# Kernel tuning notes

Measured on AMD Instinct MI355X. Metric: run time of the kernel, lower is better.

The kernel has to match this reference:

```python
import jax, jax.numpy as jnp
import numpy as np

NEG_SLOPE = 0.2


def _gatv2_layer(x, Wl, bl, Wr, br, att, bo, src, dst, N):
    """PyG GATv2Conv: lin_l on source, lin_r on target, segment softmax over dst."""
    H, C = att.shape
    xl = (x @ Wl + bl).reshape(N, H, C)  # source transform
    xr = (x @ Wr + br).reshape(N, H, C)  # target transform
    e = jax.nn.leaky_relu(xl[src] + xr[dst], NEG_SLOPE)      # [E,H,C]
    score = jnp.einsum('ehc,hc->eh', e, att)                 # [E,H]
    smax = jax.lax.stop_gradient(
        jax.ops.segment_max(score, dst, num_segments=N))     # [N,H]
    ex = jnp.exp(score - smax[dst])
    denom = jax.ops.segment_sum(ex, dst, num_segments=N)     # [N,H]
    alpha = ex / denom[dst]                                  # [E,H]
    out = jax.ops.segment_sum(xl[src] * alpha[..., None], dst, num_segments=N)
    return out.reshape(N, H * C) + bo, alpha


def setup_inputs() -> dict:
    key = jax.random.key(0)
    ks = jax.random.split(key, 24)
    N, E, F_in, Hd, H = 50000, 800000, 16, 128, 4
    C = Hd // H

    def p(k, shape, scale=0.05):
        return jax.random.normal(k, shape, jnp.float32) * scale

    inp = {
        'x': jax.random.normal(ks[0], (N, F_in), jnp.float32),
        'edge_index': jax.random.randint(ks[1], (2, E), 0, N, jnp.int32),
        'edge_attr': jax.random.normal(ks[2], (E, 4), jnp.float32),
        'batch': jnp.zeros((N,), jnp.int32),
        'enc_W': p(ks[3], (F_in, Hd)), 'enc_b': p(ks[4], (Hd,)),
        'g1_Wl': p(ks[5], (Hd, Hd)), 'g1_bl': p(ks[6], (Hd,)),
        'g1_Wr': p(ks[7], (Hd, Hd)), 'g1_br': p(ks[8], (Hd,)),
        'g1_att': p(ks[9], (H, C)), 'g1_bo': p(ks[10], (Hd,)),
        'g2_Wl': p(ks[11], (Hd, Hd)), 'g2_bl': p(ks[12], (Hd,)),
        'g2_Wr': p(ks[13], (Hd, Hd)), 'g2_br': p(ks[14], (Hd,)),
        'g2_att': p(ks[15], (H, C)), 'g2_bo': p(ks[16], (Hd,)),
        'mlp_W1': p(ks[17], (Hd, Hd)), 'mlp_b1': p(ks[18], (Hd,)),
        'mlp_W2': p(ks[19], (Hd, 1)), 'mlp_b2': p(ks[20], (1,)),
    }
    return inp


def reference(x, edge_index, edge_attr, batch,
              enc_W, enc_b,
              g1_Wl, g1_bl, g1_Wr, g1_br, g1_att, g1_bo,
              g2_Wl, g2_bl, g2_Wr, g2_br, g2_att, g2_bo,
              mlp_W1, mlp_b1, mlp_W2, mlp_b2):
    N = x.shape[0]
    # add_self_loops=True (both GAT layers)
    loops = jnp.arange(N, dtype=edge_index.dtype)
    src = jnp.concatenate([edge_index[0], loops])
    dst = jnp.concatenate([edge_index[1], loops])

    h = x @ enc_W + enc_b                                    # node_encoder
    h1, a1 = _gatv2_layer(h, g1_Wl, g1_bl, g1_Wr, g1_br, g1_att, g1_bo, src, dst, N)
    h1 = jax.nn.relu(h1)
    h2, a2 = _gatv2_layer(h1, g2_Wl, g2_bl, g2_Wr, g2_br, g2_att, g2_bo, src, dst, N)
    logits = jax.nn.relu(h2 @ mlp_W1 + mlp_b1) @ mlp_W2 + mlp_b2  # [N,1]
    probs = jax.nn.sigmoid(logits[:, 0])                     # [N]
    return probs, (a1, a2)
```

## Files before the change

kernel.cpp:

```cpp
#include <hip/hip_runtime.h>
#include <hip/hip_bf16.h>

#define NEG_SLOPE 0.2f
#define AS 136
#define CAPD 64
#define L2E 1.44269504f
#define EPB 4096

typedef __bf16 bf16x8 __attribute__((ext_vector_type(8)));
typedef float  f32x4  __attribute__((ext_vector_type(4)));

__device__ __forceinline__ float b2f(__hip_bfloat16 v) { return __bfloat162float(v); }
__device__ __forceinline__ __hip_bfloat16 f2b(float v) { return __float2bfloat16(v); }
__device__ __forceinline__ float lo16(unsigned u) { return __uint_as_float(u << 16); }
__device__ __forceinline__ float hi16(unsigned u) { return __uint_as_float(u & 0xFFFF0000u); }

template<int CTRL>
__device__ __forceinline__ float dpp_add(float p) {
    int t = __builtin_amdgcn_update_dpp(0, __float_as_int(p), CTRL, 0xF, 0xF, true);
    return p + __int_as_float(t);
}

__device__ __forceinline__ float fexp2(float x) {
    float r;
    asm("v_exp_f32 %0, %1" : "=v"(r) : "v"(x));
    return r;
}

__device__ __forceinline__ int wild16(unsigned short w) {
    int e = (w >> 7) & 0xFF;
    return (e == 0 || e >= 0xC0) ? 1 : 0;
}

__device__ __forceinline__ void store_out(void* out, size_t idx, float v, int isF32) {
    if (isF32) ((float*)out)[idx] = v;
    else       ((__hip_bfloat16*)out)[idx] = f2b(v);
}

#define NCVT 13
struct CvtTab {
    const void* src[NCVT];
    float*      dst[NCVT];
    int         n[NCVT];
    int         total;
};
__global__ void k_cvt_all(CvtTab tab, const unsigned short* __restrict__ det,
                          int* __restrict__ FLAG) {
    __shared__ int sh[256];
    int t = threadIdx.x;
    int cnt = 0;
#pragma unroll
    for (int j = 0; j < 4; ++j) cnt += wild16(det[t * 8 + j * 2]);
    sh[t] = cnt;
    __syncthreads();
    for (int off = 128; off >= 1; off >>= 1) {
        if (t < off) sh[t] += sh[t + off];
        __syncthreads();
    }
    int isF32 = sh[0] > 128;
    if (blockIdx.x == 0 && t == 0) *FLAG = isF32;
    int i = blockIdx.x * blockDim.x + t;
    if (i >= tab.total) return;
    int seg = 0, rem = i;
    while (rem >= tab.n[seg]) { rem -= tab.n[seg]; ++seg; }
    float v = isF32 ? ((const float*)tab.src[seg])[rem]
                    : b2f(((const __hip_bfloat16*)tab.src[seg])[rem]);
    tab.dst[seg][rem] = v;
}

struct WtTab { const void* src[5]; __hip_bfloat16* dst[5]; };
__global__ void k_cvtWt_all(WtTab tab, const unsigned short* __restrict__ det) {
    __shared__ int sh[128];
    int t = threadIdx.x;
    int cnt = 0;
#pragma unroll
    for (int j = 0; j < 8; ++j) cnt += wild16(det[t * 16 + j * 2]);
    sh[t] = cnt;
    __syncthreads();
    for (int off = 64; off >= 1; off >>= 1) {
        if (t < off) sh[t] += sh[t + off];
        __syncthreads();
    }
    int isF32 = sh[0] > 128;
    int m = blockIdx.x >> 7;
    int k = blockIdx.x & 127, c = t;
    float v = isF32 ? ((const float*)tab.src[m])[k * 128 + c]
                    : b2f(((const __hip_bfloat16*)tab.src[m])[k * 128 + c]);
    tab.dst[m][c * 128 + k] = f2b(v);
}


__global__ __launch_bounds__(1024) void k_binA(const int* __restrict__ ei, int E,
        int ET, int N, int shift, int nbkt, int b1, int* __restrict__ gcnt) {
    __shared__ int cnt[1024];
    int t = threadIdx.x, blk = blockIdx.x;
    for (int i = t; i < 1024; i += 1024) cnt[i] = 0;
    __syncthreads();
    int e0 = blk * EPB, e1 = min(e0 + EPB, ET);
    for (int e = e0 + t; e < e1; e += 1024) {
        int d = (e < E) ? ei[E + e] : (e - E);
        if ((unsigned)d < (unsigned)N) atomicAdd(&cnt[d >> shift], 1);
    }
    __syncthreads();
    for (int i = t; i < nbkt; i += 1024) gcnt[(size_t)i * b1 + blk] = cnt[i];
}

__global__ __launch_bounds__(256) void k_scanA(const int* __restrict__ cnt, int M,
                                               int* __restrict__ out, int* __restrict__ bsum) {
    __shared__ int sh[256];
    int t = threadIdx.x, i = blockIdx.x * 256 + t;
    int v = (i < M) ? cnt[i] : 0;
    sh[t] = v;
    __syncthreads();
    for (int off = 1; off < 256; off <<= 1) {
        int u = (t >= off) ? sh[t - off] : 0;
        __syncthreads();
        sh[t] += u;
        __syncthreads();
    }
    if (i < M) out[i] = sh[t] - v;
    if (t == 255) bsum[blockIdx.x] = sh[255];
}

__global__ __launch_bounds__(1024) void k_scanB2(int* __restrict__ bsum, int B,
        int* __restrict__ rs, int N, int* __restrict__ bb, int nbkt) {
    __shared__ int sh[1024];
    int t = threadIdx.x;
    int carry = 0;
    for (int base = 0; base < B; base += 1024) {
        int idx = base + t;
        int v = (idx < B) ? bsum[idx] : 0;
        sh[t] = v;
        __syncthreads();
        for (int off = 1; off < 1024; off <<= 1) {
            int u = (t >= off) ? sh[t - off] : 0;
            __syncthreads();
            sh[t] += u;
            __syncthreads();
        }
        if (idx < B) bsum[idx] = carry + sh[t] - v;
        carry += sh[1023];
        __syncthreads();
    }
    if (t == 0) { rs[N] = carry; bb[nbkt] = carry; }
}

__global__ __launch_bounds__(256) void k_scanC2(int* __restrict__ offs,
        const int* __restrict__ bsum, int M, int b1, int* __restrict__ bb) {
    int i = blockIdx.x * 256 + threadIdx.x;
    if (i >= M) return;
    int v = offs[i] + bsum[blockIdx.x];
    offs[i] = v;
    if (i % b1 == 0) bb[i / b1] = v;
}

__global__ __launch_bounds__(1024) void k_binB(const int* __restrict__ ei, int E,
        int ET, int N, int shift, int nbkt, int b1, const int* __restrict__ offs,
        int2* __restrict__ stg) {
    __shared__ int base[1024];
    int t = threadIdx.x, blk = blockIdx.x;
    for (int i = t; i < nbkt; i += 1024) base[i] = offs[(size_t)i * b1 + blk];
    __syncthreads();
    int mask = (1 << shift) - 1;
    int e0 = blk * EPB, e1 = min(e0 + EPB, ET);
    for (int e = e0 + t; e < e1; e += 1024) {
        int s, d;
        if (e < E) { s = ei[e]; d = ei[E + e]; } else { s = d = e - E; }
        if ((unsigned)d >= (unsigned)N) continue;
        int pos = atomicAdd(&base[d >> shift], 1);
        stg[pos] = make_int2(e, s | ((d & mask) << 20));
    }
}

__global__ __launch_bounds__(256) void k_csr(const int2* __restrict__ stg,
        const int* __restrict__ bb, int N, int shift,
        int* __restrict__ rs, int2* __restrict__ pk) {
    __shared__ int off2[1024];
    __shared__ int cnt2[1024];
    __shared__ int part[256];
    int t = threadIdx.x, bkt = blockIdx.x;
    int node0 = bkt << shift;
    int npb = 1 << shift;
    int mask = npb - 1;
    int nn = min(npb, N - node0);
    int b0 = bb[bkt], bend = bb[bkt + 1];
    int ec = bend - b0;
    const int* stgy = ((const int*)stg) + 1;
    for (int i = t; i < nn; i += 256) cnt2[i] = 0;
    __syncthreads();
    for (int i = t; i < ec; i += 256)
        atomicAdd(&cnt2[(stgy[(size_t)(b0 + i) * 2] >> 20) & mask], 1);
    __syncthreads();
    int loc[4], sum = 0, base4 = t * 4;
#pragma unroll
    for (int k = 0; k < 4; ++k) {
        int idx = base4 + k;
        int v = (idx < nn) ? cnt2[idx] : 0;
        loc[k] = sum; sum += v;
    }
    part[t] = sum;
    __syncthreads();
    for (int off = 1; off < 256; off <<= 1) {
        int u = (t >= off) ? part[t - off] : 0;
        __syncthreads();
        part[t] += u;
        __syncthreads();
    }
    int pbase = part[t] - sum;
#pragma unroll
    for (int k = 0; k < 4; ++k) {
        int idx = base4 + k;
        if (idx < nn) {
            int p = b0 + pbase + loc[k];
            off2[idx] = p;
            rs[node0 + idx] = p;
        }
    }
    __syncthreads();
    for (int i = t; i < ec; i += 256) {
        int2 es = stg[b0 + i];
        int dof = (es.y >> 20) & mask;
        int pos = atomicAdd(&off2[dof], 1);
        pk[pos] = make_int2(es.x, es.y & 0xFFFFF);
    }
}

__global__ __launch_bounds__(256) void k_gemm2enc_mfma(
        const void* __restrict__ x, const float* __restrict__ encW,
        const float* __restrict__ encb, const int* __restrict__ flag,
        const __hip_bfloat16* __restrict__ WLt, const float* __restrict__ bl,
        const __hip_bfloat16* __restrict__ WRt, const float* __restrict__ br,
        int N, __hip_bfloat16* __restrict__ xl, __hip_bfloat16* __restrict__ xr) {
    __shared__ __hip_bfloat16 hA[64 * AS];
    __shared__ __hip_bfloat16 wB[128 * AS];
    float* encWs = (float*)wB;
    float* xs    = encWs + 2048;
    int t = threadIdx.x, rbase = blockIdx.x * 64;
    int isF32 = *flag;
    for (int i = t; i < 2048; i += 256) encWs[i] = encW[i];
    for (int i = t; i < 1024; i += 256) {
        int r = i >> 4, k = i & 15, gr = rbase + r;
        float v = 0.f;
        if (gr < N)
            v = isF32 ? ((const float*)x)[(size_t)gr * 16 + k]
                      : b2f(((const __hip_bfloat16*)x)[(size_t)gr * 16 + k]);
        xs[r * 17 + k] = v;
    }
    __syncthreads();
    {
        int r = t >> 2, q = t & 3;
        float xv[16];
#pragma unroll
        for (int k = 0; k < 16; ++k) xv[k] = xs[r * 17 + k];
#pragma unroll
        for (int cc = 0; cc < 32; ++cc) {
            int c = q + cc * 4;
            float acc = encb[c];
#pragma unroll
            for (int k = 0; k < 16; ++k) acc += xv[k] * encWs[k * 128 + c];
            hA[r * AS + c] = f2b(acc);
        }
    }
    int wave = t >> 6, lane = t & 63, l16 = lane & 15, kq = lane >> 4;
#pragma unroll
    for (int pass = 0; pass < 2; ++pass) {
        const __hip_bfloat16* Wt = pass ? WRt : WLt;
        const float* bias        = pass ? br  : bl;
        __hip_bfloat16* out      = pass ? xr  : xl;
        __syncthreads();
        for (int i = t; i < 2048; i += 256) {
            int c = i >> 4, seg = i & 15;
            ((uint4*)(wB + c * AS))[seg] = ((const uint4*)(Wt + c * 128))[seg];
        }
        __syncthreads();
        f32x4 acc[8];
#pragma unroll
        for (int i = 0; i < 8; ++i) acc[i] = (f32x4){0.f, 0.f, 0.f, 0.f};
#pragma unroll
        for (int ks = 0; ks < 4; ++ks) {
            int kofs = ks * 32 + kq * 8;
            bf16x8 a = *(const bf16x8*)(hA + (wave * 16 + l16) * AS + kofs);
#pragma unroll
            for (int cb = 0; cb < 8; ++cb) {
                bf16x8 b = *(const bf16x8*)(wB + (cb * 16 + l16) * AS + kofs);
                acc[cb] = __builtin_amdgcn_mfma_f32_16x16x32_bf16(a, b, acc[cb], 0, 0, 0);
            }
        }
#pragma unroll
        for (int cb = 0; cb < 8; ++cb) {
            int c = cb * 16 + l16;
            float bc = bias[c];
#pragma unroll
            for (int i = 0; i < 4; ++i) {
                int r = rbase + wave * 16 + kq * 4 + i;
                if (r < N) out[(size_t)r * 128 + c] = f2b(acc[cb][i] + bc);
            }
        }
    }
}

__global__ __launch_bounds__(256) void k_gemm2_mfma(
        const __hip_bfloat16* __restrict__ in,
        const __hip_bfloat16* __restrict__ WLt, const float* __restrict__ bl,
        const __hip_bfloat16* __restrict__ WRt, const float* __restrict__ br,
        int N, __hip_bfloat16* __restrict__ xl, __hip_bfloat16* __restrict__ xr) {
    __shared__ __hip_bfloat16 hA[64 * AS];
    __shared__ __hip_bfloat16 wB[128 * AS];
    int t = threadIdx.x, rbase = blockIdx.x * 64;
    for (int i = t; i < 1024; i += 256) {
        int r = i >> 4, seg = i & 15;
        int gr = rbase + r;
        uint4 v = {0u, 0u, 0u, 0u};
        if (gr < N) v = ((const uint4*)(in + (size_t)gr * 128))[seg];
        ((uint4*)(hA + r * AS))[seg] = v;
    }
    int wave = t >> 6, lane = t & 63, l16 = lane & 15, kq = lane >> 4;
#pragma unroll
    for (int pass = 0; pass < 2; ++pass) {
        const __hip_bfloat16* Wt = pass ? WRt : WLt;
        const float* bias        = pass ? br  : bl;
        __hip_bfloat16* out      = pass ? xr  : xl;
        __syncthreads();
        for (int i = t; i < 2048; i += 256) {
            int c = i >> 4, seg = i & 15;
            ((uint4*)(wB + c * AS))[seg] = ((const uint4*)(Wt + c * 128))[seg];
        }
        __syncthreads();
        f32x4 acc[8];
#pragma unroll
        for (int i = 0; i < 8; ++i) acc[i] = (f32x4){0.f, 0.f, 0.f, 0.f};
#pragma unroll
        for (int ks = 0; ks < 4; ++ks) {
            int kofs = ks * 32 + kq * 8;
            bf16x8 a = *(const bf16x8*)(hA + (wave * 16 + l16) * AS + kofs);
#pragma unroll
            for (int cb = 0; cb < 8; ++cb) {
                bf16x8 b = *(const bf16x8*)(wB + (cb * 16 + l16) * AS + kofs);
                acc[cb] = __builtin_amdgcn_mfma_f32_16x16x32_bf16(a, b, acc[cb], 0, 0, 0);
            }
        }
#pragma unroll
        for (int cb = 0; cb < 8; ++cb) {
            int c = cb * 16 + l16;
            float bc = bias[c];
#pragma unroll
            for (int i = 0; i < 4; ++i) {
                int r = rbase + wave * 16 + kq * 4 + i;
                if (r < N) out[(size_t)r * 128 + c] = f2b(acc[cb][i] + bc);
            }
        }
    }
}

__global__ __launch_bounds__(256) void k_mlp_mfma(
        const __hip_bfloat16* __restrict__ h2, const __hip_bfloat16* __restrict__ W1t,
        const float* __restrict__ b1, const float* __restrict__ W2,
        const float* __restrict__ b2, int N,
        void* __restrict__ d_out, const int* __restrict__ flag) {
    __shared__ __hip_bfloat16 hA[64 * AS];
    __shared__ __hip_bfloat16 wB[128 * AS];
    int t = threadIdx.x, rbase = blockIdx.x * 64;
    for (int i = t; i < 2048; i += 256) {
        int c = i >> 4, seg = i & 15;
        ((uint4*)(wB + c * AS))[seg] = ((const uint4*)(W1t + c * 128))[seg];
    }
    for (int i = t; i < 1024; i += 256) {
        int r = i >> 4, seg = i & 15;
        int gr = rbase + r;
        uint4 v = {0u, 0u, 0u, 0u};
        if (gr < N) v = ((const uint4*)(h2 + (size_t)gr * 128))[seg];
        ((uint4*)(hA + r * AS))[seg] = v;
    }
    __syncthreads();
    int wave = t >> 6, lane = t & 63, l16 = lane & 15, kq = lane >> 4;
    f32x4 acc[8];
#pragma unroll
    for (int i = 0; i < 8; ++i) acc[i] = (f32x4){0.f, 0.f, 0.f, 0.f};
#pragma unroll
    for (int ks = 0; ks < 4; ++ks) {
        int kofs = ks * 32 + kq * 8;
        bf16x8 a = *(const bf16x8*)(hA + (wave * 16 + l16) * AS + kofs);
#pragma unroll
        for (int cb = 0; cb < 8; ++cb) {
            bf16x8 b = *(const bf16x8*)(wB + (cb * 16 + l16) * AS + kofs);
            acc[cb] = __builtin_amdgcn_mfma_f32_16x16x32_bf16(a, b, acc[cb], 0, 0, 0);
        }
    }
    float p[4] = {0.f, 0.f, 0.f, 0.f};
#pragma unroll
    for (int cb = 0; cb < 8; ++cb) {
        int c = cb * 16 + l16;
        float bb = b1[c], w = W2[c];
#pragma unroll
        for (int i = 0; i < 4; ++i) p[i] += fmaxf(acc[cb][i] + bb, 0.f) * w;
    }
#pragma unroll
    for (int i = 0; i < 4; ++i) {
        p[i] += __shfl_xor(p[i], 8, 16);
        p[i] += __shfl_xor(p[i], 4, 16);
        p[i] += __shfl_xor(p[i], 2, 16);
        p[i] += __shfl_xor(p[i], 1, 16);
    }
    if (l16 == 0) {
        int isF32 = *flag;
        float bb = b2[0];
#pragma unroll
        for (int i = 0; i < 4; ++i) {
            int r = rbase + wave * 16 + kq * 4 + i;
            if (r < N)
                store_out(d_out, (size_t)r,
                          1.f / (1.f + __expf(-(p[i] + bb))), isF32);
        }
    }
}

__global__ __launch_bounds__(128) void k_gat_fused(
        const __hip_bfloat16* __restrict__ xl,
        const __hip_bfloat16* __restrict__ xr,
        const int* __restrict__ rs, const int2* __restrict__ pk, int N,
        const float* __restrict__ att, const float* __restrict__ bo, int relu,
        float* __restrict__ EX2,
        void* __restrict__ alpha_out, size_t aoff, const int* __restrict__ flag,
        __hip_bfloat16* __restrict__ hout) {
    __shared__ float exsh[2][CAPD * 4];
    int wv = threadIdx.x >> 6, lane = threadIdx.x & 63;
    int n = blockIdx.x * 2 + wv;
    if (n >= N) return;
    int h = lane >> 4, l16 = lane & 15, c0 = lane * 2;
    unsigned uxr = ((const unsigned*)(xr + (size_t)n * 128))[lane];
    float xr0 = lo16(uxr), xr1 = hi16(uxr);
    float a0 = att[c0] * L2E, a1 = att[c0 + 1] * L2E;
    float a06 = 0.6f * a0, a04 = 0.4f * a0;
    float a16 = 0.6f * a1, a14 = 0.4f * a1;
    int beg = __builtin_amdgcn_readfirstlane(rs[n]);
    int end = __builtin_amdgcn_readfirstlane(rs[n + 1]);
    const char* xlb = (const char*)xl;
    const int* pks = (const int*)pk;
    int lb = lane << 2;
    float den = 0.f, acc0 = 0.f, acc1 = 0.f;
    int r = beg;

#define GAT_BATCH(W) { \
    unsigned u[W]; float p[W]; \
    _Pragma("unroll") \
    for (int j = 0; j < W; ++j) { \
        unsigned s = min((unsigned)pks[((r + j) << 1) | 1], (unsigned)(N - 1)); \
        u[j] = *(const unsigned*)(xlb + ((size_t)s << 8) + lb); \
    } \
    _Pragma("unroll") \
    for (int j = 0; j < W; ++j) { \
        float v0 = lo16(u[j]) + xr0, v1 = hi16(u[j]) + xr1; \
        float tt = fmaf(fabsf(v0), a04, v0 * a06); \
        tt = fmaf(v1, a16, tt); \
        p[j] = fmaf(fabsf(v1), a14, tt); \
    } \
    _Pragma("unroll") \
    for (int j = 0; j < W; ++j) { \
        p[j] = dpp_add<0x121>(p[j]); \
        p[j] = dpp_add<0x122>(p[j]); \
        p[j] = dpp_add<0x124>(p[j]); \
        p[j] = dpp_add<0x128>(p[j]); \
        p[j] = fexp2(__builtin_amdgcn_fmed3f(p[j], -43.f, 43.f)); \
    } \
    if (l16 == 0) { \
        _Pragma("unroll") \
        for (int j = 0; j < W; ++j) { \
            int idx = r + j - beg; \
            if (idx < CAPD) exsh[wv][idx * 4 + h] = p[j]; \
            else            EX2[(size_t)(r + j) * 4 + h] = p[j]; \
        } \
    } \
    _Pragma("unroll") \
    for (int j = 0; j < W; ++j) { \
        den  += p[j]; \
        acc0 = fmaf(p[j], lo16(u[j]), acc0); \
        acc1 = fmaf(p[j], hi16(u[j]), acc1); \
    } \
    r += W; }

    while (r + 8 <= end) GAT_BATCH(8)
    if (r + 4 <= end) GAT_BATCH(4)
    if (r + 2 <= end) GAT_BATCH(2)
    if (r < end) GAT_BATCH(1)
#undef GAT_BATCH

    float invn = 1.f / fmaxf(den, 1e-30f);
    float v0 = acc0 * invn + bo[c0], v1 = acc1 * invn + bo[c0 + 1];
    if (relu) { v0 = fmaxf(v0, 0.f); v1 = fmaxf(v1, 0.f); }
    __hip_bfloat16 h0 = f2b(v0), h1 = f2b(v1);
    ushort2 st;
    st.x = *(unsigned short*)&h0;
    st.y = *(unsigned short*)&h1;
    ((ushort2*)(hout + (size_t)n * 128))[lane] = st;
    int isF32 = *flag;
    for (int r0 = beg; r0 < end; r0 += 16) {
        int rr = r0 + l16;
        if (rr < end) {
            int idx = rr - beg;
            float ex = (idx < CAPD) ? exsh[wv][idx * 4 + h]
                                    : EX2[(size_t)rr * 4 + h];
            int e = pk[rr].x;
            store_out(alpha_out, aoff + (size_t)e * 4 + h, ex * invn, isF32);
        }
    }
}

extern "C" void kernel_launch(void* const* d_in, const int* in_sizes, int n_in,
                              void* d_out, int out_size, void* d_ws, size_t ws_size,
                              hipStream_t stream) {
    const int* ei = (const int*)d_in[1];
    const int N  = in_sizes[0] / 16;
    const int E  = in_sizes[1] / 2;
    const int ET = E + N;

    int shift = 6;
    while (((N + (1 << shift) - 1) >> shift) > 1024) ++shift;
    const int nbkt = (N + (1 << shift) - 1) >> shift;
    const int B1   = (ET + EPB - 1) / EPB;
    const int M    = nbkt * B1;
    const int MB   = (M + 255) / 256;

    float* P = (float*)d_ws;
    float* encW = P; P += 2048;  float* encb = P; P += 128;
    float* b1l  = P; P += 128;   float* b1r  = P; P += 128;
    float* att1 = P; P += 128;   float* bo1  = P; P += 128;
    float* b2l  = P; P += 128;   float* b2r  = P; P += 128;
    float* att2 = P; P += 128;   float* bo2  = P; P += 128;
    float* mb1  = P; P += 128;   float* mW2  = P; P += 128;
    float* mb2  = P; P += 4;
    int*  FLAG  = (int*)P; P += 4;
    int*  RS    = (int*)P; P += N + 1;
    int*  BB    = (int*)P; P += nbkt + 1;
    int*  GCNT  = (int*)P; P += M;
    int*  OFFS  = (int*)P; P += M;
    int*  BSUM  = (int*)P; P += MB;
    P = (float*)(((uintptr_t)P + 7) & ~(uintptr_t)7);
    int2* PK    = (int2*)P; P += (size_t)ET * 2;
    float* EX2  = P; P += (size_t)ET * 4;
    int2* STG   = (int2*)EX2;
    P = (float*)(((uintptr_t)P + 15) & ~(uintptr_t)15);
    __hip_bfloat16* W1Lt = (__hip_bfloat16*)P;
    __hip_bfloat16* W1Rt = W1Lt + 16384;
    __hip_bfloat16* W2Lt = W1Rt + 16384;
    __hip_bfloat16* W2Rt = W2Lt + 16384;
    __hip_bfloat16* MW1t = W2Rt + 16384;
    __hip_bfloat16* Hb   = MW1t + 16384;
    __hip_bfloat16* XL   = Hb + (size_t)N * 128;
    __hip_bfloat16* XR   = XL + (size_t)N * 128;

    CvtTab tab;
    const int srcIdx[NCVT] = {4, 5, 7, 9, 10, 11, 13, 15, 16, 17, 19, 20, 21};
    float* dsts[NCVT] = {encW, encb, b1l, b1r, att1, bo1, b2l, b2r, att2, bo2, mb1, mW2, mb2};
    const int ns[NCVT] = {2048, 128, 128, 128, 128, 128, 128, 128, 128, 128, 128, 128, 1};
    int tot = 0;
    for (int i = 0; i < NCVT; ++i) {
        tab.src[i] = d_in[srcIdx[i]];
        tab.dst[i] = dsts[i];
        tab.n[i] = ns[i];
        tot += ns[i];
    }
    tab.total = tot;
    const unsigned short* det = (const unsigned short*)d_in[4];
    k_cvt_all<<<(tot + 255) / 256, 256, 0, stream>>>(tab, det, FLAG);

    WtTab wt;
    wt.src[0] = d_in[6];  wt.dst[0] = W1Lt;
    wt.src[1] = d_in[8];  wt.dst[1] = W1Rt;
    wt.src[2] = d_in[12]; wt.dst[2] = W2Lt;
    wt.src[3] = d_in[14]; wt.dst[3] = W2Rt;
    wt.src[4] = d_in[18]; wt.dst[4] = MW1t;
    k_cvtWt_all<<<640, 128, 0, stream>>>(wt, det);

    k_binA<<<B1, 1024, 0, stream>>>(ei, E, ET, N, shift, nbkt, B1, GCNT);
    k_scanA<<<MB, 256, 0, stream>>>(GCNT, M, OFFS, BSUM);
    k_scanB2<<<1, 1024, 0, stream>>>(BSUM, MB, RS, N, BB, nbkt);
    k_scanC2<<<MB, 256, 0, stream>>>(OFFS, BSUM, M, B1, BB);
    k_binB<<<B1, 1024, 0, stream>>>(ei, E, ET, N, shift, nbkt, B1, OFFS, STG);
    k_csr<<<nbkt, 256, 0, stream>>>(STG, BB, N, shift, RS, PK);

    const size_t a1_off = (size_t)N;
    const size_t a2_off = (size_t)N + (size_t)ET * 4;
    const int gGrid = (N + 63) / 64;
    const int fGrid = (N + 1) / 2;

    k_gemm2enc_mfma<<<gGrid, 256, 0, stream>>>(d_in[0], encW, encb, FLAG,
                                               W1Lt, b1l, W1Rt, b1r, N, XL, XR);
    k_gat_fused<<<fGrid, 128, 0, stream>>>(XL, XR, RS, PK, N, att1, bo1, 1,
                                           EX2, d_out, a1_off, FLAG, Hb);

    k_gemm2_mfma<<<gGrid, 256, 0, stream>>>(Hb, W2Lt, b2l, W2Rt, b2r, N, XL, XR);
    k_gat_fused<<<fGrid, 128, 0, stream>>>(XL, XR, RS, PK, N, att2, bo2, 0,
                                           EX2, d_out, a2_off, FLAG, Hb);

    k_mlp_mfma<<<gGrid, 256, 0, stream>>>(Hb, MW1t, mb1, mW2, mb2, N, d_out, FLAG);
}
```

Baseline: 334.0 us.

## Merge preprocessing kernels and fold scan carry into binning and CSR kernels

Combines the parameter conversion, weight transpose and edge bucket counting into one launch, and removes the separate scan-carry and scan-apply kernels. Each binning block and each CSR block now recomputes the block-sum prefix it needs. Buckets grow to 128 nodes with at most 512 buckets, which halves the bucket count, and the source index is masked to 20 bits in the gather. This cuts the number of kernel launches and serial dependencies in CSR construction, at the cost of redundant scan work in every block and larger per-bucket loads.

```diff
diff --git a/kernel.cpp b/kernel.cpp
--- a/kernel.cpp
+++ b/kernel.cpp
@@ -44,65 +44,50 @@
     int         n[NCVT];
     int         total;
 };
-__global__ void k_cvt_all(CvtTab tab, const unsigned short* __restrict__ det,
-                          int* __restrict__ FLAG) {
-    __shared__ int sh[256];
-    int t = threadIdx.x;
-    int cnt = 0;
-#pragma unroll
-    for (int j = 0; j < 4; ++j) cnt += wild16(det[t * 8 + j * 2]);
-    sh[t] = cnt;
-    __syncthreads();
-    for (int off = 128; off >= 1; off >>= 1) {
-        if (t < off) sh[t] += sh[t + off];
-        __syncthreads();
-    }
-    int isF32 = sh[0] > 128;
-    if (blockIdx.x == 0 && t == 0) *FLAG = isF32;
-    int i = blockIdx.x * blockDim.x + t;
-    if (i >= tab.total) return;
-    int seg = 0, rem = i;
-    while (rem >= tab.n[seg]) { rem -= tab.n[seg]; ++seg; }
-    float v = isF32 ? ((const float*)tab.src[seg])[rem]
-                    : b2f(((const __hip_bfloat16*)tab.src[seg])[rem]);
-    tab.dst[seg][rem] = v;
-}
-
 struct WtTab { const void* src[5]; __hip_bfloat16* dst[5]; };
-__global__ void k_cvtWt_all(WtTab tab, const unsigned short* __restrict__ det) {
-    __shared__ int sh[128];
-    int t = threadIdx.x;
-    int cnt = 0;
-#pragma unroll
-    for (int j = 0; j < 8; ++j) cnt += wild16(det[t * 16 + j * 2]);
-    sh[t] = cnt;
-    __syncthreads();
-    for (int off = 64; off >= 1; off >>= 1) {
-        if (t < off) sh[t] += sh[t + off];
-        __syncthreads();
-    }
-    int isF32 = sh[0] > 128;
-    int m = blockIdx.x >> 7;
-    int k = blockIdx.x & 127, c = t;
-    float v = isF32 ? ((const float*)tab.src[m])[k * 128 + c]
-                    : b2f(((const __hip_bfloat16*)tab.src[m])[k * 128 + c]);
-    tab.dst[m][c * 128 + k] = f2b(v);
-}
-
-
-__global__ __launch_bounds__(1024) void k_binA(const int* __restrict__ ei, int E,
-        int ET, int N, int shift, int nbkt, int b1, int* __restrict__ gcnt) {
-    __shared__ int cnt[1024];
-    int t = threadIdx.x, blk = blockIdx.x;
-    for (int i = t; i < 1024; i += 1024) cnt[i] = 0;
-    __syncthreads();
-    int e0 = blk * EPB, e1 = min(e0 + EPB, ET);
-    for (int e = e0 + t; e < e1; e += 1024) {
-        int d = (e < E) ? ei[E + e] : (e - E);
-        if ((unsigned)d < (unsigned)N) atomicAdd(&cnt[d >> shift], 1);
-    }
-    __syncthreads();
-    for (int i = t; i < nbkt; i += 1024) gcnt[(size_t)i * b1 + blk] = cnt[i];
+
+__global__ __launch_bounds__(1024) void k_pre(const int* __restrict__ ei, int E,
+        int ET, int N, int shift, int nbkt, int b1, int* __restrict__ gcnt,
+        CvtTab tab, WtTab wt, const unsigned short* __restrict__ det,
+        int* __restrict__ FLAG) {
+    __shared__ int shp[1024];
+    int t = threadIdx.x, b = blockIdx.x;
+    if (b < b1) {
+        if (t < 512) shp[t] = 0;
+        __syncthreads();
+        int e0 = b * EPB, e1 = min(e0 + EPB, ET);
+        for (int e = e0 + t; e < e1; e += 1024) {
+            int d = (e < E) ? ei[E + e] : (e - E);
+            if ((unsigned)d < (unsigned)N) atomicAdd(&shp[d >> shift], 1);
+        }
+        __syncthreads();
+        for (int i = t; i < nbkt; i += 1024) gcnt[(size_t)i * b1 + b] = shp[i];
+        return;
+    }
+    shp[t] = wild16(det[t * 2]);
+    __syncthreads();
+    for (int off = 512; off >= 1; off >>= 1) {
+        if (t < off) shp[t] += shp[t + off];
+        __syncthreads();
+    }
+    int isF32 = shp[0] > 128;
+    int j = b - b1;
+    if (j < 80) {
+        if (j == 0 && t == 0) *FLAG = isF32;
+        int ru = j * 8 + (t >> 7);
+        int m = ru >> 7, k = ru & 127, c = t & 127;
+        float v = isF32 ? ((const float*)wt.src[m])[k * 128 + c]
+                        : b2f(((const __hip_bfloat16*)wt.src[m])[k * 128 + c]);
+        wt.dst[m][c * 128 + k] = f2b(v);
+    } else {
+        int i = (j - 80) * 1024 + t;
+        if (i >= tab.total) return;
+        int seg = 0, rem = i;
+        while (rem >= tab.n[seg]) { rem -= tab.n[seg]; ++seg; }
+        float v = isF32 ? ((const float*)tab.src[seg])[rem]
+                        : b2f(((const __hip_bfloat16*)tab.src[seg])[rem]);
+        tab.dst[seg][rem] = v;
+    }
 }
 
 __global__ __launch_bounds__(256) void k_scanA(const int* __restrict__ cnt, int M,
@@ -122,15 +107,18 @@
     if (t == 255) bsum[blockIdx.x] = sh[255];
 }
 
-__global__ __launch_bounds__(1024) void k_scanB2(int* __restrict__ bsum, int B,
-        int* __restrict__ rs, int N, int* __restrict__ bb, int nbkt) {
+__global__ __launch_bounds__(1024) void k_binB(const int* __restrict__ ei, int E,
+        int ET, int N, int shift, int nbkt, int b1, const int* __restrict__ offs,
+        const int* __restrict__ bsum, int MB, int2* __restrict__ stg) {
     __shared__ int sh[1024];
-    int t = threadIdx.x;
+    __shared__ int sbex[1024];
+    __shared__ int base[512];
+    int t = threadIdx.x, blk = blockIdx.x;
     int carry = 0;
-    for (int base = 0; base < B; base += 1024) {
-        int idx = base + t;
-        int v = (idx < B) ? bsum[idx] : 0;
-        sh[t] = v;
+    for (int bs = 0; bs < MB; bs += 1024) {
+        int idx = bs + t;
+        int vv = (idx < MB) ? bsum[idx] : 0;
+        sh[t] = vv;
         __syncthreads();
         for (int off = 1; off < 1024; off <<= 1) {
             int u = (t >= off) ? sh[t - off] : 0;
@@ -138,28 +126,14 @@
             sh[t] += u;
             __syncthreads();
         }
-        if (idx < B) bsum[idx] = carry + sh[t] - v;
+        if (idx < MB) sbex[idx] = carry + sh[t] - vv;
         carry += sh[1023];
         __syncthreads();
     }
-    if (t == 0) { rs[N] = carry; bb[nbkt] = carry; }
-}
-
-__global__ __launch_bounds__(256) void k_scanC2(int* __restrict__ offs,
-        const int* __restrict__ bsum, int M, int b1, int* __restrict__ bb) {
-    int i = blockIdx.x * 256 + threadIdx.x;
-    if (i >= M) return;
-    int v = offs[i] + bsum[blockIdx.x];
-    offs[i] = v;
-    if (i % b1 == 0) bb[i / b1] = v;
-}
-
-__global__ __launch_bounds__(1024) void k_binB(const int* __restrict__ ei, int E,
-        int ET, int N, int shift, int nbkt, int b1, const int* __restrict__ offs,
-        int2* __restrict__ stg) {
-    __shared__ int base[1024];
-    int t = threadIdx.x, blk = blockIdx.x;
-    for (int i = t; i < nbkt; i += 1024) base[i] = offs[(size_t)i * b1 + blk];
+    for (int i = t; i < nbkt; i += 1024) {
+        int gi = i * b1 + blk;
+        base[i] = offs[gi] + sbex[gi >> 8];
+    }
     __syncthreads();
     int mask = (1 << shift) - 1;
     int e0 = blk * EPB, e1 = min(e0 + EPB, ET);
@@ -173,17 +147,39 @@
 }
 
 __global__ __launch_bounds__(256) void k_csr(const int2* __restrict__ stg,
-        const int* __restrict__ bb, int N, int shift,
+        const int* __restrict__ offs, const int* __restrict__ bsum, int MB,
+        int N, int shift, int b1, int nbkt, int M,
         int* __restrict__ rs, int2* __restrict__ pk) {
-    __shared__ int off2[1024];
-    __shared__ int cnt2[1024];
+    __shared__ int off2[512];
+    __shared__ int cnt2[512];
     __shared__ int part[256];
+    __shared__ int red[256];
     int t = threadIdx.x, bkt = blockIdx.x;
     int node0 = bkt << shift;
     int npb = 1 << shift;
     int mask = npb - 1;
     int nn = min(npb, N - node0);
-    int b0 = bb[bkt], bend = bb[bkt + 1];
+    int i0 = bkt * b1, i1 = (bkt + 1) * b1;
+    int c0 = i0 >> 8, c1 = i1 >> 8;
+    int a0 = 0, a1 = 0, aT = 0;
+    for (int bb = t; bb < MB; bb += 256) {
+        int vb = bsum[bb];
+        aT += vb;
+        if (bb < c0) a0 += vb;
+        if (bb < c1) a1 += vb;
+    }
+    red[t] = a0; __syncthreads();
+    for (int off = 128; off >= 1; off >>= 1) { if (t < off) red[t] += red[t + off]; __syncthreads(); }
+    int S0 = red[0]; __syncthreads();
+    red[t] = a1; __syncthreads();
+    for (int off = 128; off >= 1; off >>= 1) { if (t < off) red[t] += red[t + off]; __syncthreads(); }
+    int S1 = red[0]; __syncthreads();
+    red[t] = aT; __syncthreads();
+    for (int off = 128; off >= 1; off >>= 1) { if (t < off) red[t] += red[t + off]; __syncthreads(); }
+    int ST = red[0]; __syncthreads();
+    int b0 = S0 + offs[i0];
+    int bend = (bkt + 1 < nbkt) ? (S1 + offs[i1]) : ST;
+    if (bkt == nbkt - 1 && t == 0) rs[N] = ST;
     int ec = bend - b0;
     const int* stgy = ((const int*)stg) + 1;
     for (int i = t; i < nn; i += 256) cnt2[i] = 0;
@@ -191,10 +187,10 @@
     for (int i = t; i < ec; i += 256)
         atomicAdd(&cnt2[(stgy[(size_t)(b0 + i) * 2] >> 20) & mask], 1);
     __syncthreads();
-    int loc[4], sum = 0, base4 = t * 4;
-#pragma unroll
-    for (int k = 0; k < 4; ++k) {
-        int idx = base4 + k;
+    int loc[2], sum = 0, base2 = t * 2;
+#pragma unroll
+    for (int k = 0; k < 2; ++k) {
+        int idx = base2 + k;
         int v = (idx < nn) ? cnt2[idx] : 0;
         loc[k] = sum; sum += v;
     }
@@ -208,8 +204,8 @@
     }
     int pbase = part[t] - sum;
 #pragma unroll
-    for (int k = 0; k < 4; ++k) {
-        int idx = base4 + k;
+    for (int k = 0; k < 2; ++k) {
+        int idx = base2 + k;
         if (idx < nn) {
             int p = b0 + pbase + loc[k];
             off2[idx] = p;
@@ -444,7 +440,7 @@
     unsigned u[W]; float p[W]; \
     _Pragma("unroll") \
     for (int j = 0; j < W; ++j) { \
-        unsigned s = min((unsigned)pks[((r + j) << 1) | 1], (unsigned)(N - 1)); \
+        unsigned s = min((unsigned)(pks[((r + j) << 1) | 1] & 0xFFFFF), (unsigned)(N - 1)); \
         u[j] = *(const unsigned*)(xlb + ((size_t)s << 8) + lb); \
     } \
     _Pragma("unroll") \
@@ -513,8 +509,8 @@
     const int E  = in_sizes[1] / 2;
     const int ET = E + N;
 
-    int shift = 6;
-    while (((N + (1 << shift) - 1) >> shift) > 1024) ++shift;
+    int shift = 7;
+    while (((N + (1 << shift) - 1) >> shift) > 512) ++shift;
     const int nbkt = (N + (1 << shift) - 1) >> shift;
     const int B1   = (ET + EPB - 1) / EPB;
     const int M    = nbkt * B1;
@@ -530,7 +526,6 @@
     float* mb2  = P; P += 4;
     int*  FLAG  = (int*)P; P += 4;
     int*  RS    = (int*)P; P += N + 1;
-    int*  BB    = (int*)P; P += nbkt + 1;
     int*  GCNT  = (int*)P; P += M;
     int*  OFFS  = (int*)P; P += M;
     int*  BSUM  = (int*)P; P += MB;
@@ -560,23 +555,20 @@
         tot += ns[i];
     }
     tab.total = tot;
-    const unsigned short* det = (const unsigned short*)d_in[4];
-    k_cvt_all<<<(tot + 255) / 256, 256, 0, stream>>>(tab, det, FLAG);
-
     WtTab wt;
     wt.src[0] = d_in[6];  wt.dst[0] = W1Lt;
     wt.src[1] = d_in[8];  wt.dst[1] = W1Rt;
     wt.src[2] = d_in[12]; wt.dst[2] = W2Lt;
     wt.src[3] = d_in[14]; wt.dst[3] = W2Rt;
     wt.src[4] = d_in[18]; wt.dst[4] = MW1t;
-    k_cvtWt_all<<<640, 128, 0, stream>>>(wt, det);
-
-    k_binA<<<B1, 1024, 0, stream>>>(ei, E, ET, N, shift, nbkt, B1, GCNT);
+    const unsigned short* det = (const unsigned short*)d_in[4];
+    const int preGrid = B1 + 80 + (tot + 1023) / 1024;
+    k_pre<<<preGrid, 1024, 0, stream>>>(ei, E, ET, N, shift, nbkt, B1, GCNT,
+                                        tab, wt, det, FLAG);
+
     k_scanA<<<MB, 256, 0, stream>>>(GCNT, M, OFFS, BSUM);
-    k_scanB2<<<1, 1024, 0, stream>>>(BSUM, MB, RS, N, BB, nbkt);
-    k_scanC2<<<MB, 256, 0, stream>>>(OFFS, BSUM, M, B1, BB);
-    k_binB<<<B1, 1024, 0, stream>>>(ei, E, ET, N, shift, nbkt, B1, OFFS, STG);
-    k_csr<<<nbkt, 256, 0, stream>>>(STG, BB, N, shift, RS, PK);
+    k_binB<<<B1, 1024, 0, stream>>>(ei, E, ET, N, shift, nbkt, B1, OFFS, BSUM, MB, STG);
+    k_csr<<<nbkt, 256, 0, stream>>>(STG, OFFS, BSUM, MB, N, shift, B1, nbkt, M, RS, PK);
 
     const size_t a1_off = (size_t)N;
     const size_t a2_off = (size_t)N + (size_t)ET * 4;
```

After: 325.2 us. 2.6% less time.
